# Kernel optimization log

Measured on AMD Instinct MI355X. Metric: run time of the kernel, lower is better.

Reference implementation:

```python
import jax, jax.numpy as jnp
import numpy as np

B = 32768      # batch
D = 512        # embedding dim
V = 100000     # vocab_length (row 0 reserved -> table has V+1 rows)
S = 100        # num_neg_samples (hard-coded in source)
DISTORTION = 0.4


def _expected_counts():
    # fixed_unigram sampler: zipf-ish counts, distorted by 0.4, 1 reserved id
    counts = 1.0 / np.arange(1, V + 1, dtype=np.float64)
    p = counts ** DISTORTION
    p = p / p.sum()
    q = np.zeros(V + 1, dtype=np.float64)
    # unique sampling expected count: E[id in sample] = 1-(1-p)^S
    q[1:] = -np.expm1(S * np.log1p(-p))
    q[0] = 1e-9  # reserved id, never sampled; avoid log(0)
    return q


def setup_inputs() -> dict:
    key = jax.random.key(0)
    k1, k2, k3, k4 = jax.random.split(key, 4)
    label = jax.random.randint(k1, (B,), 1, V + 1, dtype=jnp.int64)
    inputs = jax.random.normal(k2, (B, D), dtype=jnp.float32)
    weights = jax.random.normal(k3, (V + 1, D), dtype=jnp.float32) * 0.05
    biases = jnp.zeros((V + 1,), dtype=jnp.float32)
    sampled_ids = jax.random.choice(k4, V, (S,), replace=False).astype(jnp.int64) + 1
    q = jnp.asarray(_expected_counts(), dtype=jnp.float32)
    true_expected_count = q[label]          # [B]
    sampled_expected_count = q[sampled_ids]  # [S]
    return {
        "label": label, "inputs": inputs, "weights": weights, "biases": biases,
        "sampled_ids": sampled_ids,
        "true_expected_count": true_expected_count,
        "sampled_expected_count": sampled_expected_count,
    }


def reference(label, inputs, weights, biases, sampled_ids,
              true_expected_count, sampled_expected_count):
    # --- _compute_sampled_logits with subtract_log_q=True ---
    true_w = weights[label]                                   # [B, D] gather
    true_logits = (jnp.einsum('bd,bd->b', inputs, true_w)
                   + biases[label]
                   - jnp.log(true_expected_count))            # [B]
    samp_w = weights[sampled_ids]                             # [S, D] gather
    samp_logits = (jnp.einsum('bd,sd->bs', inputs, samp_w)
                   + biases[sampled_ids]
                   - jnp.log(sampled_expected_count))         # [B, S]
    logits = jnp.concatenate([true_logits[:, None], samp_logits], axis=1)  # [B, 1+S]
    # labels are one-hot at column 0 -> CE = logsumexp - true logit
    losses = jax.nn.logsumexp(logits, axis=1) - logits[:, 0]
    loss = jnp.mean(losses)
    return logits, loss
```

## Files before the change

kernel.cpp:

```cpp
#include <hip/hip_runtime.h>
#include <math.h>

#define B_TOT 32768
#define DIM   512
#define NS    100
#define NCOL  101
#define TB    128
#define NBLK  (B_TOT / TB)
#define NPACK (16 * 7 * 64)

#define BASE_OFF 28672
#define LPART_OFF 28800

typedef __attribute__((ext_vector_type(8))) short short8;
typedef __attribute__((ext_vector_type(4))) float f32x4;

static __device__ __forceinline__ short f2bf(float f) {
    unsigned u = __builtin_bit_cast(unsigned, f);
    unsigned r = (u + 0x7FFFu + ((u >> 16) & 1u)) >> 16;
    return (short)r;
}

__global__ __launch_bounds__(256)
void pack_kernel(const float* __restrict__ weights, const float* __restrict__ biases,
                 const int* __restrict__ sids, const float* __restrict__ sq,
                 short* __restrict__ wpack, float* __restrict__ base_g)
{
    const int tid = blockIdx.x * 256 + threadIdx.x;
    if (tid < 112)
        base_g[tid] = (tid < NS) ? biases[sids[tid]] - logf(sq[tid]) : -INFINITY;
    if (tid >= NPACK) return;
    const int kc = tid / 448, rem = tid % 448;
    const int c = rem >> 6, l = rem & 63;
    const int col = c * 16 + (l & 15);
    const int k   = kc * 32 + (l >> 4) * 8;
    short8 v = (short8){0, 0, 0, 0, 0, 0, 0, 0};
    if (col < NS) {
        const float* src = weights + (long)sids[col] * DIM + k;
        const float4 f0 = *(const float4*)src;
        const float4 f1 = *(const float4*)(src + 4);
        v[0] = f2bf(f0.x); v[1] = f2bf(f0.y); v[2] = f2bf(f0.z); v[3] = f2bf(f0.w);
        v[4] = f2bf(f1.x); v[5] = f2bf(f1.y); v[6] = f2bf(f1.z); v[7] = f2bf(f1.w);
    }
    *(short8*)&wpack[(long)tid * 8] = v;
}

__global__ __launch_bounds__(1024, 4)
void fused_kernel(const int* __restrict__ label,
                  const float* __restrict__ inputs,
                  const float* __restrict__ weights,
                  const float* __restrict__ biases,
                  const float* __restrict__ tq,
                  const short* __restrict__ wpack,
                  const float* __restrict__ base_g,
                  float* __restrict__ out,
                  float* __restrict__ lpart)
{
    __shared__ short W_lds[NPACK * 8];
    __shared__ float tl_x[TB];
    __shared__ float ls_lds[8];

    const int t = threadIdx.x;

    {
        const short8* src = (const short8*)wpack;
        short8* dst = (short8*)W_lds;
        #pragma unroll
        for (int s = 0; s < 7; s++)
            dst[s * 1024 + t] = src[s * 1024 + t];
    }

    const int wave = t >> 6;
    const int lane = t & 63;
    const int rg   = wave >> 1;
    const int kh   = wave & 1;
    const int rit  = lane & 15;
    const int seg  = lane >> 4;
    const int absRow = blockIdx.x * TB + rg * 16 + rit;
    const int lab = label[absRow];
    const float* aptr = inputs  + (long)absRow * DIM + kh * 256 + seg * 8;
    const float* wtp  = weights + (long)lab    * DIM + kh * 256 + seg * 8;

    f32x4 acc[7];
    #pragma unroll
    for (int c = 0; c < 7; c++) acc[c] = (f32x4){0.f, 0.f, 0.f, 0.f};
    float tacc = 0.f;

    __syncthreads();

    #pragma unroll
    for (int kc = 0; kc < 8; kc++) {
        const int k0 = kc * 32;
        const float4 a0 = *(const float4*)(aptr + k0);
        const float4 a1 = *(const float4*)(aptr + k0 + 4);
        const float4 w0 = *(const float4*)(wtp + k0);
        const float4 w1 = *(const float4*)(wtp + k0 + 4);

        tacc = fmaf(a0.x, w0.x, tacc); tacc = fmaf(a0.y, w0.y, tacc);
        tacc = fmaf(a0.z, w0.z, tacc); tacc = fmaf(a0.w, w0.w, tacc);
        tacc = fmaf(a1.x, w1.x, tacc); tacc = fmaf(a1.y, w1.y, tacc);
        tacc = fmaf(a1.z, w1.z, tacc); tacc = fmaf(a1.w, w1.w, tacc);

        short8 af;
        af[0] = f2bf(a0.x); af[1] = f2bf(a0.y); af[2] = f2bf(a0.z); af[3] = f2bf(a0.w);
        af[4] = f2bf(a1.x); af[5] = f2bf(a1.y); af[6] = f2bf(a1.z); af[7] = f2bf(a1.w);

        const int kcg = kh * 8 + kc;
        const short* wp = &W_lds[((kcg * 7) * 64 + lane) * 8];
        #pragma unroll
        for (int c = 0; c < 7; c++) {
            const short8 bf = *(const short8*)(wp + c * 64 * 8);
            acc[c] = __builtin_amdgcn_mfma_f32_16x16x32_bf16(af, bf, acc[c], 0, 0, 0);
        }
    }

    tacc += __shfl_xor(tacc, 16);
    tacc += __shfl_xor(tacc, 32);

    __syncthreads();

    float* ex = (float*)W_lds;
    if (kh == 1) {
        const int base = rg * 1856 + lane * 29;
        #pragma unroll
        for (int c = 0; c < 7; c++)
            #pragma unroll
            for (int i = 0; i < 4; i++)
                ex[base + c * 4 + i] = acc[c][i];
        if (lane < 16) tl_x[rg * 16 + lane] = tacc;
    }
    __syncthreads();

    if (kh == 0) {
        const int base = rg * 1856 + lane * 29;
        #pragma unroll
        for (int c = 0; c < 7; c++)
            #pragma unroll
            for (int i = 0; i < 4; i++)
                acc[c][i] += ex[base + c * 4 + i];
        tacc += tl_x[rg * 16 + rit];

        float base_v[7];
        #pragma unroll
        for (int c = 0; c < 7; c++) base_v[c] = base_g[c * 16 + rit];

        const float tl = tacc + biases[lab] - logf(tq[absRow]);
        if (lane < 16) out[(long)absRow * NCOL] = tl;

        const int g = lane >> 4;
        float loss_sum = 0.f;
        #pragma unroll
        for (int i = 0; i < 4; i++) {
            const int r = g * 4 + i;
            const long orow = (long)(blockIdx.x * TB + rg * 16 + r) * NCOL;
            const float tlv = __shfl(tl, r);
            float v[7];
            float m = tlv;
            #pragma unroll
            for (int c = 0; c < 7; c++) {
                v[c] = acc[c][i] + base_v[c];
                m = fmaxf(m, v[c]);
            }
            #pragma unroll
            for (int off = 1; off < 16; off <<= 1) m = fmaxf(m, __shfl_xor(m, off));
            float s = (rit == 0) ? expf(tlv - m) : 0.f;
            #pragma unroll
            for (int c = 0; c < 7; c++) s += expf(v[c] - m);
            #pragma unroll
            for (int off = 1; off < 16; off <<= 1) s += __shfl_xor(s, off);
            loss_sum += m + logf(s) - tlv;
            #pragma unroll
            for (int c = 0; c < 7; c++) {
                const int col = c * 16 + rit;
                if (col < NS) out[orow + 1 + col] = v[c];
            }
        }
        float wl = (rit == 0) ? loss_sum : 0.f;
        wl += __shfl_xor(wl, 16);
        wl += __shfl_xor(wl, 32);
        if (lane == 0) ls_lds[rg] = wl;
    }
    __syncthreads();
    if (t == 0) {
        float bp = 0.f;
        #pragma unroll
        for (int w = 0; w < 8; w++) bp += ls_lds[w];
        lpart[blockIdx.x] = bp;
    }
}

__global__ __launch_bounds__(256)
void reduce_kernel(const float* __restrict__ lpart, float* __restrict__ out_loss)
{
    __shared__ double buf[256];
    buf[threadIdx.x] = (double)lpart[threadIdx.x];
    __syncthreads();
    for (int o = 128; o > 0; o >>= 1) {
        if (threadIdx.x < o) buf[threadIdx.x] += buf[threadIdx.x + o];
        __syncthreads();
    }
    if (threadIdx.x == 0) *out_loss = (float)(buf[0] * (1.0 / (double)B_TOT));
}

extern "C" void kernel_launch(void* const* d_in, const int* in_sizes, int n_in,
                              void* d_out, int out_size, void* d_ws, size_t ws_size,
                              hipStream_t stream)
{
    const int*   label   = (const int*)d_in[0];
    const float* inputs  = (const float*)d_in[1];
    const float* weights = (const float*)d_in[2];
    const float* biases  = (const float*)d_in[3];
    const int*   sids    = (const int*)d_in[4];
    const float* tq      = (const float*)d_in[5];
    const float* sq      = (const float*)d_in[6];
    float* out  = (float*)d_out;
    float* ws_f = (float*)d_ws;
    short* wpack  = (short*)d_ws;
    float* base_g = ws_f + BASE_OFF;
    float* lpart  = ws_f + LPART_OFF;

    pack_kernel<<<28, 256, 0, stream>>>(weights, biases, sids, sq, wpack, base_g);
    fused_kernel<<<NBLK, 1024, 0, stream>>>(label, inputs, weights, biases, tq,
                                            wpack, base_g, out, lpart);
    reduce_kernel<<<1, 256, 0, stream>>>(lpart, out + (long)B_TOT * NCOL);
}
```

Measured before the change: 41.40 us.

## Specialize waves: half do full-K MFMA, half compute true-label dot products

Waves are no longer split over K halves with an LDS exchange of partial accumulators. Eight waves now run the full 512-wide MFMA over all 16 K-chunks, and the other eight waves compute the true-label dot product with coalesced float4 loads, writing the true logit to LDS. This removes the partial-sum exchange and one barrier. In exchange the MFMA waves each do twice the serial K work, and the two wave groups may not finish at the same time.

```diff
diff --git a/kernel.cpp b/kernel.cpp
--- a/kernel.cpp
+++ b/kernel.cpp
@@ -57,7 +57,7 @@
                   float* __restrict__ lpart)
 {
     __shared__ short W_lds[NPACK * 8];
-    __shared__ float tl_x[TB];
+    __shared__ float tl_lds[TB];
     __shared__ float ls_lds[8];
 
     const int t = threadIdx.x;
@@ -72,88 +72,81 @@
 
     const int wave = t >> 6;
     const int lane = t & 63;
-    const int rg   = wave >> 1;
-    const int kh   = wave & 1;
-    const int rit  = lane & 15;
-    const int seg  = lane >> 4;
-    const int absRow = blockIdx.x * TB + rg * 16 + rit;
-    const int lab = label[absRow];
-    const float* aptr = inputs  + (long)absRow * DIM + kh * 256 + seg * 8;
-    const float* wtp  = weights + (long)lab    * DIM + kh * 256 + seg * 8;
+    const long b0 = (long)blockIdx.x * TB;
+
+    __syncthreads();
 
     f32x4 acc[7];
     #pragma unroll
     for (int c = 0; c < 7; c++) acc[c] = (f32x4){0.f, 0.f, 0.f, 0.f};
-    float tacc = 0.f;
-
-    __syncthreads();
-
-    #pragma unroll
-    for (int kc = 0; kc < 8; kc++) {
-        const int k0 = kc * 32;
-        const float4 a0 = *(const float4*)(aptr + k0);
-        const float4 a1 = *(const float4*)(aptr + k0 + 4);
-        const float4 w0 = *(const float4*)(wtp + k0);
-        const float4 w1 = *(const float4*)(wtp + k0 + 4);
-
-        tacc = fmaf(a0.x, w0.x, tacc); tacc = fmaf(a0.y, w0.y, tacc);
-        tacc = fmaf(a0.z, w0.z, tacc); tacc = fmaf(a0.w, w0.w, tacc);
-        tacc = fmaf(a1.x, w1.x, tacc); tacc = fmaf(a1.y, w1.y, tacc);
-        tacc = fmaf(a1.z, w1.z, tacc); tacc = fmaf(a1.w, w1.w, tacc);
-
-        short8 af;
-        af[0] = f2bf(a0.x); af[1] = f2bf(a0.y); af[2] = f2bf(a0.z); af[3] = f2bf(a0.w);
-        af[4] = f2bf(a1.x); af[5] = f2bf(a1.y); af[6] = f2bf(a1.z); af[7] = f2bf(a1.w);
-
-        const int kcg = kh * 8 + kc;
-        const short* wp = &W_lds[((kcg * 7) * 64 + lane) * 8];
-        #pragma unroll
-        for (int c = 0; c < 7; c++) {
-            const short8 bf = *(const short8*)(wp + c * 64 * 8);
-            acc[c] = __builtin_amdgcn_mfma_f32_16x16x32_bf16(af, bf, acc[c], 0, 0, 0);
-        }
-    }
-
-    tacc += __shfl_xor(tacc, 16);
-    tacc += __shfl_xor(tacc, 32);
-
-    __syncthreads();
-
-    float* ex = (float*)W_lds;
-    if (kh == 1) {
-        const int base = rg * 1856 + lane * 29;
-        #pragma unroll
-        for (int c = 0; c < 7; c++)
-            #pragma unroll
-            for (int i = 0; i < 4; i++)
-                ex[base + c * 4 + i] = acc[c][i];
-        if (lane < 16) tl_x[rg * 16 + lane] = tacc;
-    }
-    __syncthreads();
-
-    if (kh == 0) {
-        const int base = rg * 1856 + lane * 29;
-        #pragma unroll
-        for (int c = 0; c < 7; c++)
-            #pragma unroll
-            for (int i = 0; i < 4; i++)
-                acc[c][i] += ex[base + c * 4 + i];
-        tacc += tl_x[rg * 16 + rit];
-
+
+    if (wave >= 8) {
+        const int rg = wave - 8;
+        const int rr = lane >> 2;
+        const int j  = lane & 3;
+        const long absRow = b0 + rg * 16 + rr;
+        const int lab = label[absRow];
+        const float* ap = inputs  + absRow * DIM + j * 4;
+        const float* wp = weights + (long)lab * DIM + j * 4;
+        float t0 = 0.f, t1 = 0.f;
+        #pragma unroll
+        for (int i = 0; i < 32; i += 2) {
+            const float4 a0 = *(const float4*)(ap + i * 16);
+            const float4 w0 = *(const float4*)(wp + i * 16);
+            const float4 a1 = *(const float4*)(ap + (i + 1) * 16);
+            const float4 w1 = *(const float4*)(wp + (i + 1) * 16);
+            t0 = fmaf(a0.x, w0.x, t0); t0 = fmaf(a0.y, w0.y, t0);
+            t0 = fmaf(a0.z, w0.z, t0); t0 = fmaf(a0.w, w0.w, t0);
+            t1 = fmaf(a1.x, w1.x, t1); t1 = fmaf(a1.y, w1.y, t1);
+            t1 = fmaf(a1.z, w1.z, t1); t1 = fmaf(a1.w, w1.w, t1);
+        }
+        float tacc = t0 + t1;
+        tacc += __shfl_xor(tacc, 1);
+        tacc += __shfl_xor(tacc, 2);
+        if (j == 0) {
+            const float tl = tacc + biases[lab] - logf(tq[absRow]);
+            tl_lds[rg * 16 + rr] = tl;
+            out[absRow * NCOL] = tl;
+        }
+    } else {
+        const int rg  = wave;
+        const int rit = lane & 15;
+        const int seg = lane >> 4;
+        const float* aptr = inputs + (b0 + rg * 16 + rit) * DIM + seg * 8;
+
+        #pragma unroll
+        for (int kc = 0; kc < 16; kc++) {
+            const int k0 = kc * 32;
+            const float4 a0 = *(const float4*)(aptr + k0);
+            const float4 a1 = *(const float4*)(aptr + k0 + 4);
+            short8 af;
+            af[0] = f2bf(a0.x); af[1] = f2bf(a0.y); af[2] = f2bf(a0.z); af[3] = f2bf(a0.w);
+            af[4] = f2bf(a1.x); af[5] = f2bf(a1.y); af[6] = f2bf(a1.z); af[7] = f2bf(a1.w);
+            const short* wp = &W_lds[((kc * 7) * 64 + lane) * 8];
+            #pragma unroll
+            for (int c = 0; c < 7; c++) {
+                const short8 bf = *(const short8*)(wp + c * 64 * 8);
+                acc[c] = __builtin_amdgcn_mfma_f32_16x16x32_bf16(af, bf, acc[c], 0, 0, 0);
+            }
+        }
+    }
+
+    __syncthreads();
+
+    if (wave < 8) {
+        const int rg  = wave;
+        const int rit = lane & 15;
+        const int g   = lane >> 4;
         float base_v[7];
         #pragma unroll
         for (int c = 0; c < 7; c++) base_v[c] = base_g[c * 16 + rit];
 
-        const float tl = tacc + biases[lab] - logf(tq[absRow]);
-        if (lane < 16) out[(long)absRow * NCOL] = tl;
-
-        const int g = lane >> 4;
         float loss_sum = 0.f;
         #pragma unroll
         for (int i = 0; i < 4; i++) {
             const int r = g * 4 + i;
-            const long orow = (long)(blockIdx.x * TB + rg * 16 + r) * NCOL;
-            const float tlv = __shfl(tl, r);
+            const long orow = (b0 + rg * 16 + r) * NCOL;
+            const float tlv = tl_lds[rg * 16 + r];
             float v[7];
             float m = tlv;
             #pragma unroll
```

Result: slower. 44.26 us (+6.9%).
